# Kernel tuning notes

Hardware: AMD Instinct MI355X
Metric: run time of the kernel (lower is better)

## Reference

```python
import jax, jax.numpy as jnp
import numpy as np
import math

B, S, E, H = 2, 8192, 1024, 16
D = E // H  # 64
CHUNK = 128


def _build_slopes(n):
    # ALiBi-style slopes (n is a power of 2 here)
    start = 2.0 ** (-(2.0 ** -(math.log2(n) - 3)))
    return np.array([start * (start ** i) for i in range(n)], dtype=np.float32)


def setup_inputs() -> dict:
    key = jax.random.key(0)
    ks = jax.random.split(key, 6)
    x = jax.random.normal(ks[0], (B, S, E), dtype=jnp.float32)
    # rotary table: (S, D//2, 2) = (cos, sin)
    inv_freq = 1.0 / (10000.0 ** (np.arange(0, D, 2, dtype=np.float32) / D))
    ang = np.arange(S, dtype=np.float32)[:, None] * inv_freq[None, :]  # (S, D/2)
    freqs_cis = jnp.asarray(np.stack([np.cos(ang), np.sin(ang)], axis=-1))
    wq = jax.random.normal(ks[1], (E, E), dtype=jnp.float32) * 0.02
    wk = jax.random.normal(ks[2], (E, E), dtype=jnp.float32) * 0.02
    wv = jax.random.normal(ks[3], (E, E), dtype=jnp.float32) * 0.02
    wo = jax.random.normal(ks[4], (E, E), dtype=jnp.float32) * 0.02
    rms_w = jnp.ones((E,), dtype=jnp.float32)
    return {"x": x, "freqs_cis": freqs_cis, "wq": wq, "wk": wk, "wv": wv, "wo": wo, "rms_w": rms_w}


def apply_rotary(x, fc):
    # x: (b, s, h, d); fc: (s, d/2, 2)
    xr = x.reshape(*x.shape[:-1], -1, 2)          # (b,s,h,d/2,2)
    fc = fc[None, :, None, :, :]                   # (1,s,1,d/2,2)
    out = jnp.stack([
        xr[..., 0] * fc[..., 0] - xr[..., 1] * fc[..., 1],
        xr[..., 1] * fc[..., 0] + xr[..., 0] * fc[..., 1],
    ], axis=-1)
    return out.reshape(x.shape)


def lightning_attn(q, k, v, slopes, C=CHUNK):
    # q,k,v: (B,H,S,D); per-head decay lambda = exp(-slope)
    Bs, Hs, Ss, Ds = q.shape
    NC = Ss // C
    j = jnp.arange(C, dtype=jnp.float32)
    diff = j[:, None] - j[None, :]
    s3 = slopes[:, None, None]                     # (H,1,1)
    Dmask = jnp.where(diff >= 0, jnp.exp(-s3 * diff), 0.0)   # (H,C,C) intra decay
    q_dec = jnp.exp(-slopes[:, None] * (j + 1.0))             # (H,C) cross-chunk q decay
    k_dec = jnp.exp(-slopes[:, None] * (C - 1.0 - j))         # (H,C) state-update k decay
    c_dec = jnp.exp(-slopes * C)[None, :, None, None]         # (1,H,1,1) full-chunk decay
    qc = q.reshape(Bs, Hs, NC, C, Ds).transpose(2, 0, 1, 3, 4)
    kc = k.reshape(Bs, Hs, NC, C, Ds).transpose(2, 0, 1, 3, 4)
    vc = v.reshape(Bs, Hs, NC, C, Ds).transpose(2, 0, 1, 3, 4)

    def step(St, inp):
        qb, kb, vb = inp                                       # (B,H,C,D)
        scores = jnp.einsum('bhid,bhjd->bhij', qb, kb) * Dmask[None]
        o = jnp.einsum('bhij,bhjd->bhid', scores, vb)
        o = o + q_dec[None, :, :, None] * jnp.einsum('bhid,bhde->bhie', qb, St)
        St = c_dec * St + jnp.einsum('bhcd,bhce->bhde', kb * k_dec[None, :, :, None], vb)
        return St, o

    S0 = jnp.zeros((Bs, Hs, Ds, Ds), dtype=jnp.float32)
    _, oc = jax.lax.scan(step, S0, (qc, kc, vc))               # oc: (NC,B,H,C,D)
    return oc.transpose(1, 2, 0, 3, 4).reshape(Bs, Hs, Ss, Ds)


def rms_norm(x, w, eps=1e-5):
    xf = x.astype(jnp.float32)
    n = xf * jax.lax.rsqrt(jnp.mean(xf * xf, axis=-1, keepdims=True) + eps)
    return n.astype(x.dtype) * w


def reference(x, freqs_cis, wq, wk, wv, wo, rms_w):
    b, s, _ = x.shape
    slopes = jnp.asarray(_build_slopes(H))
    q = (x @ wq.T).reshape(b, s, H, D)
    k = (x @ wk.T).reshape(b, s, H, D)
    v = (x @ wv.T).reshape(b, s, H, D)
    q = apply_rotary(q, freqs_cis)
    k = apply_rotary(k, freqs_cis)
    q = q.transpose(0, 2, 1, 3)   # (B,H,S,D)
    k = k.transpose(0, 2, 1, 3)
    v = v.transpose(0, 2, 1, 3)
    o = lightning_attn(q, k, v, slopes)             # (B,H,S,D)
    o = o.transpose(0, 2, 1, 3).reshape(b, s, E)    # b n (h d)
    o = rms_norm(o, rms_w)
    return o @ wo.T
```

## Files before the change

kernel.cpp:

```cpp
#include <hip/hip_runtime.h>


using h16   = _Float16;
using h16x8 = __attribute__((ext_vector_type(8))) _Float16;
using h16x4 = __attribute__((ext_vector_type(4))) _Float16;
using f32x4 = __attribute__((ext_vector_type(4))) float;

#define MFMA16(a,b,c) __builtin_amdgcn_mfma_f32_16x16x32_f16(a,b,c,0,0,0)

#define GLOAD16(gp, lp) __builtin_amdgcn_global_load_lds( \
    (const __attribute__((address_space(1))) void*)(gp),  \
    (__attribute__((address_space(3))) void*)(lp), 16, 0, 0)

__device__ __forceinline__ h16x8 rope8(h16x8 v, const float* __restrict__ fp) {
  float4 f0 = *(const float4*)fp;
  float4 f1 = *(const float4*)(fp + 4);
  h16x8 o; float x0, x1;
  x0=(float)v[0]; x1=(float)v[1]; o[0]=(h16)(x0*f0.x - x1*f0.y); o[1]=(h16)(x1*f0.x + x0*f0.y);
  x0=(float)v[2]; x1=(float)v[3]; o[2]=(h16)(x0*f0.z - x1*f0.w); o[3]=(h16)(x1*f0.z + x0*f0.w);
  x0=(float)v[4]; x1=(float)v[5]; o[4]=(h16)(x0*f1.x - x1*f1.y); o[5]=(h16)(x1*f1.x + x0*f1.y);
  x0=(float)v[6]; x1=(float)v[7]; o[6]=(h16)(x0*f1.z - x1*f1.w); o[7]=(h16)(x1*f1.z + x0*f1.w);
  return o;
}

__global__ __launch_bounds__(256) void k_cvt(const float* __restrict__ s,
                                             h16* __restrict__ d, int n) {
  int i = (blockIdx.x * 256 + threadIdx.x) * 8;
  if (i >= n) return;
  float4 a = *(const float4*)(s + i);
  float4 b = *(const float4*)(s + i + 4);
  h16x8 o;
  o[0]=(h16)a.x; o[1]=(h16)a.y; o[2]=(h16)a.z; o[3]=(h16)a.w;
  o[4]=(h16)b.x; o[5]=(h16)b.y; o[6]=(h16)b.z; o[7]=(h16)b.w;
  *(h16x8*)(d + i) = o;
}

__device__ __forceinline__ void gemm256_loop(
    const h16* __restrict__ At, const h16* __restrict__ Bt,
    char* smem, int w, int l, f32x4 (&acc)[8][4])
{
  const int tid = w*64 + l;
  const int wr = w >> 2, wc = w & 3;

  size_t gof[2];
  #pragma unroll
  for (int c = 0; c < 2; c++) {
    int G = c*512 + tid;
    int pp = G >> 3;
    int idx = (G & 7) ^ (pp & 7);
    gof[c] = (size_t)(2*pp + (idx >> 2))*1024 + (idx & 3)*8;
  }

  const int q16 = ((((l & 1) << 2) | (l >> 4)) ^ ((l >> 1) & 7)) * 16;
  const int abyte = wr*8192 + ((l >> 1) & 7)*128 + q16;
  const int bbyte = 16384 + wc*4096 + ((l >> 1) & 7)*128 + q16;

  auto stageA = [&](int kt) {
    char* buf = smem + (kt & 3)*32768;
    #pragma unroll
    for (int c = 0; c < 2; c++)
      GLOAD16(At + gof[c] + kt*32, buf + c*8192 + w*1024);
  };
  auto stageB = [&](int kt) {
    char* buf = smem + (kt & 3)*32768;
    #pragma unroll
    for (int c = 0; c < 2; c++)
      GLOAD16(Bt + gof[c] + kt*32, buf + 16384 + c*8192 + w*1024);
  };

  stageA(0); stageB(0); stageA(1); stageB(1);
  asm volatile("s_waitcnt vmcnt(4)" ::: "memory");
  __builtin_amdgcn_sched_barrier(0);
  __builtin_amdgcn_s_barrier();

  for (int t = 0; t < 32; ++t) {
    const char* buf = smem + (t & 3)*32768;
    h16x8 af[8], bf[4];
    #pragma unroll
    for (int mf = 0; mf < 4; mf++) af[mf] = *(const h16x8*)(buf + abyte + mf*1024);
    #pragma unroll
    for (int nf = 0; nf < 4; nf++) bf[nf] = *(const h16x8*)(buf + bbyte + nf*1024);
    if (t < 30) stageA(t + 2);
    asm volatile("s_waitcnt lgkmcnt(0)" ::: "memory");
    __builtin_amdgcn_sched_barrier(0);
    __builtin_amdgcn_s_setprio(1);
    #pragma unroll
    for (int mf = 0; mf < 4; mf++)
      #pragma unroll
      for (int nf = 0; nf < 4; nf++)
        acc[mf][nf] = MFMA16(af[mf], bf[nf], acc[mf][nf]);
    __builtin_amdgcn_s_setprio(0);
    #pragma unroll
    for (int mf = 0; mf < 4; mf++) af[4+mf] = *(const h16x8*)(buf + abyte + 4096 + mf*1024);
    if (t < 30) stageB(t + 2);
    asm volatile("s_waitcnt lgkmcnt(0)" ::: "memory");
    __builtin_amdgcn_sched_barrier(0);
    __builtin_amdgcn_s_setprio(1);
    #pragma unroll
    for (int mf = 0; mf < 4; mf++)
      #pragma unroll
      for (int nf = 0; nf < 4; nf++)
        acc[4+mf][nf] = MFMA16(af[4+mf], bf[nf], acc[4+mf][nf]);
    __builtin_amdgcn_s_setprio(0);
    if (t < 30)       asm volatile("s_waitcnt vmcnt(4)" ::: "memory");
    else if (t == 30) asm volatile("s_waitcnt vmcnt(0)" ::: "memory");
    if (t < 31) {
      __builtin_amdgcn_sched_barrier(0);
      __builtin_amdgcn_s_barrier();
    }
  }
}

__global__ __launch_bounds__(512, 2) void k_qkv(
    const h16* __restrict__ xh, const h16* __restrict__ w3,
    h16* __restrict__ qn, h16* __restrict__ kn, h16* __restrict__ vn)
{
  extern __shared__ __align__(16) char smem[];
  const int tid = threadIdx.x;
  const int w = tid >> 6, l = tid & 63;
  const int m0 = blockIdx.x * 256;
  const int nt = blockIdx.y;
  const int wr = w >> 2, wc = w & 3;

  f32x4 acc[8][4] = {};
  gemm256_loop(xh + (size_t)m0*1024, w3 + (size_t)(nt*256)*1024, smem, w, l, acc);

  const int proj = nt >> 2;
  h16* dst = proj == 0 ? qn : (proj == 1 ? kn : vn);
  const int cb = (nt & 3)*256 + wc*64;
  #pragma unroll
  for (int mf = 0; mf < 8; mf++)
    #pragma unroll
    for (int nf = 0; nf < 4; nf++)
      #pragma unroll
      for (int r = 0; r < 4; r++) {
        int row = wr*128 + mf*16 + ((l >> 4) << 2) + r;
        int col = cb + nf*16 + (l & 15);
        dst[(size_t)(m0 + row)*1024 + col] = (h16)acc[mf][nf][r];
      }
}

__global__ __launch_bounds__(512, 2) void k_out(
    const h16* __restrict__ an, const h16* __restrict__ woh,
    float* __restrict__ out)
{
  extern __shared__ __align__(16) char smem[];
  const int tid = threadIdx.x;
  const int w = tid >> 6, l = tid & 63;
  const int m0 = blockIdx.x * 256;
  const int n0 = blockIdx.y * 256;
  const int wr = w >> 2, wc = w & 3;

  f32x4 acc[8][4] = {};
  gemm256_loop(an + (size_t)m0*1024, woh + (size_t)n0*1024, smem, w, l, acc);

  #pragma unroll
  for (int mf = 0; mf < 8; mf++)
    #pragma unroll
    for (int nf = 0; nf < 4; nf++)
      #pragma unroll
      for (int r = 0; r < 4; r++) {
        int row = wr*128 + mf*16 + ((l >> 4) << 2) + r;
        int col = n0 + wc*64 + nf*16 + (l & 15);
        out[(size_t)(m0 + row)*1024 + col] = acc[mf][nf][r];
      }
}

__global__ __launch_bounds__(256) void k_tr(
    const h16* __restrict__ kn, const h16* __restrict__ vn,
    const float* __restrict__ fc,
    h16* __restrict__ kts, h16* __restrict__ vt)
{
  __shared__ __align__(16) h16 tl[128*64];
  __shared__ float dt[128];
  const int tid = threadIdx.x;
  const int st = blockIdx.x;
  const int bh = blockIdx.y;
  const int b = bh >> 4, h = bh & 15;
  if (tid < 128) {
    float slope = exp2f(-0.5f * (float)(h + 1));
    dt[tid] = expf(-slope * (float)(127 - tid));
  }
  const size_t ibase = ((size_t)(b*8192 + st*128))*1024 + h*64;
  const size_t obase = (size_t)bh*64*8192 + st*128;
  const int cr = tid >> 3, c8 = tid & 7;

  for (int which = 0; which < 2; ++which) {
    const h16* src = which ? vn : kn;
    h16* dstp = which ? vt : kts;
    __syncthreads();
    #pragma unroll
    for (int i = 0; i < 4; i++) {
      int r = i*32 + cr;
      h16x8 v = *(const h16x8*)(src + ibase + (size_t)r*1024 + c8*8);
      if (!which) v = rope8(v, fc + (size_t)(st*128 + r)*64 + c8*8);
      int slot = (c8 + ((r >> 3) & 7)) & 7;
      *(h16x8*)(tl + r*64 + slot*8) = v;
    }
    __syncthreads();
    #pragma unroll
    for (int i = 0; i < 4; i++) {
      int chunk = i*256 + tid;
      int d = chunk >> 4;
      int j8 = chunk & 15;
      h16x8 o;
      #pragma unroll
      for (int jj = 0; jj < 8; jj++) {
        int c = j8*8 + jj;
        int pos = (d + ((c >> 3) & 7)*8) & 63;
        float fv = (float)tl[c*64 + pos];
        if (!which) fv *= dt[c];
        o[jj] = (h16)fv;
      }
      *(h16x8*)(dstp + obase + (size_t)d*8192 + j8*8) = o;
    }
  }
}

__global__ __launch_bounds__(256) void k_kv(
    const h16* __restrict__ kts, const h16* __restrict__ vt,
    float* __restrict__ T)
{
  const int tid = threadIdx.x;
  const int t = blockIdx.x;
  const int bh = blockIdx.y;
  const int w = tid >> 6, l = tid & 63;
  const h16* vb = vt  + (size_t)bh*64*8192 + t*128;
  const h16* kb = kts + (size_t)bh*64*8192 + t*128;
  f32x4 acc[4] = {};
  h16x8 a[4];
  #pragma unroll
  for (int ks = 0; ks < 4; ks++)
    a[ks] = *(const h16x8*)(vb + (size_t)(w*16 + (l & 15))*8192 + ks*32 + (l >> 4)*8);
  #pragma unroll
  for (int nf = 0; nf < 4; nf++) {
    #pragma unroll
    for (int ks = 0; ks < 4; ks++) {
      h16x8 bfr = *(const h16x8*)(kb + (size_t)(nf*16 + (l & 15))*8192 + ks*32 + (l >> 4)*8);
      acc[nf] = MFMA16(a[ks], bfr, acc[nf]);
    }
  }
  float* Tb = T + ((size_t)bh*64 + t)*4096;
  #pragma unroll
  for (int nf = 0; nf < 4; nf++)
    #pragma unroll
    for (int r = 0; r < 4; r++) {
      int e = w*16 + ((l >> 4) << 2) + r;
      int d = nf*16 + (l & 15);
      Tb[e*64 + d] = acc[nf][r];
    }
}

__global__ __launch_bounds__(256) void k_scan(const float* __restrict__ T,
                                              h16* __restrict__ ph) {
  const int bh = blockIdx.x;
  const int j  = blockIdx.y * 256 + threadIdx.x;
  const int h = bh & 15;
  const float cdec = expf(-exp2f(-0.5f*(float)(h+1)) * 128.0f);
  const float* Tb = T + (size_t)bh*64*4096 + j;
  h16* pb = ph + (size_t)bh*64*4096 + j;
  float run = 0.f;
  for (int t = 0; t < 64; t++) {
    float kv = Tb[(size_t)t*4096];
    pb[(size_t)t*4096] = (h16)run;
    run = cdec*run + kv;
  }
}

__global__ __launch_bounds__(256) void k_att(
    const h16* __restrict__ qn, const h16* __restrict__ kn,
    const float* __restrict__ fc,
    const h16* __restrict__ vt, const h16* __restrict__ ph,
    h16* __restrict__ oh)
{
  __shared__ __align__(16) h16 P[128*144];
  __shared__ float dt[128], qd[128];
  const int tid = threadIdx.x;
  const int t = blockIdx.x;
  const int bh = blockIdx.y;
  const int b = bh >> 4, h = bh & 15;
  if (tid < 128) {
    float slope = exp2f(-0.5f*(float)(h+1));
    dt[tid] = expf(-slope*(float)tid);
    qd[tid] = expf(-slope*(float)(tid+1));
  }
  __syncthreads();
  const int w = tid >> 6, l = tid & 63;
  const int iw = w * 32;
  const h16* qb = qn + ((size_t)(b*8192 + t*128))*1024 + h*64;
  const h16* kb = kn + ((size_t)(b*8192 + t*128))*1024 + h*64;
  const h16* vb = vt + (size_t)bh*64*8192 + t*128;
  const h16* pb = ph + ((size_t)bh*64 + t)*4096;
  const float* fcb = fc + (size_t)(t*128)*64;

  h16x8 aq[2][2];
  #pragma unroll
  for (int mf = 0; mf < 2; mf++)
    #pragma unroll
    for (int ks = 0; ks < 2; ks++) {
      int row = iw + mf*16 + (l & 15);
      int d0 = ks*32 + (l >> 4)*8;
      aq[mf][ks] = rope8(*(const h16x8*)(qb + (size_t)row*1024 + d0),
                         fcb + (size_t)row*64 + d0);
    }

  f32x4 sc[2][8] = {};
  #pragma unroll
  for (int nf = 0; nf < 8; nf++) {
    if (nf*16 <= iw + 31) {
      #pragma unroll
      for (int ks = 0; ks < 2; ks++) {
        int row = nf*16 + (l & 15);
        int d0 = ks*32 + (l >> 4)*8;
        h16x8 bk = rope8(*(const h16x8*)(kb + (size_t)row*1024 + d0),
                         fcb + (size_t)row*64 + d0);
        sc[0][nf] = MFMA16(aq[0][ks], bk, sc[0][nf]);
        sc[1][nf] = MFMA16(aq[1][ks], bk, sc[1][nf]);
      }
    }
  }
  #pragma unroll
  for (int mf = 0; mf < 2; mf++) {
    #pragma unroll
    for (int nf = 0; nf < 8; nf++) {
      #pragma unroll
      for (int r = 0; r < 4; r++) {
        int i = iw + mf*16 + ((l >> 4) << 2) + r;
        int j = nf*16 + (l & 15);
        int diff = i - j;
        float v = diff >= 0 ? sc[mf][nf][r]*dt[diff] : 0.f;
        P[i*144 + j] = (h16)v;
      }
    }
  }
  f32x4 ao[2][4] = {};
  #pragma unroll
  for (int kc = 0; kc < 4; kc++) {
    h16x8 ap0 = *(const h16x8*)(P + (size_t)(iw + (l & 15))*144 + kc*32 + (l >> 4)*8);
    h16x8 ap1 = *(const h16x8*)(P + (size_t)(iw + 16 + (l & 15))*144 + kc*32 + (l >> 4)*8);
    #pragma unroll
    for (int nf = 0; nf < 4; nf++) {
      h16x8 bv = *(const h16x8*)(vb + (size_t)(nf*16 + (l & 15))*8192 + kc*32 + (l >> 4)*8);
      ao[0][nf] = MFMA16(ap0, bv, ao[0][nf]);
      ao[1][nf] = MFMA16(ap1, bv, ao[1][nf]);
    }
  }
  f32x4 a2[2][4] = {};
  #pragma unroll
  for (int ks = 0; ks < 2; ks++) {
    #pragma unroll
    for (int nf = 0; nf < 4; nf++) {
      h16x8 bs = *(const h16x8*)(pb + (size_t)(nf*16 + (l & 15))*64 + ks*32 + (l >> 4)*8);
      a2[0][nf] = MFMA16(aq[0][ks], bs, a2[0][nf]);
      a2[1][nf] = MFMA16(aq[1][ks], bs, a2[1][nf]);
    }
  }
  #pragma unroll
  for (int mf = 0; mf < 2; mf++) {
    #pragma unroll
    for (int nf = 0; nf < 4; nf++) {
      #pragma unroll
      for (int r = 0; r < 4; r++) {
        int i = iw + mf*16 + ((l >> 4) << 2) + r;
        int e = nf*16 + (l & 15);
        float o = ao[mf][nf][r] + qd[i]*a2[mf][nf][r];
        int s = t*128 + i;
        oh[((size_t)(b*8192 + s))*1024 + h*64 + e] = (h16)o;
      }
    }
  }
}

__global__ __launch_bounds__(256) void k_rms(const h16* __restrict__ o,
                                             const float* __restrict__ rw,
                                             h16* __restrict__ an) {
  const int tid = threadIdx.x;
  const size_t base = (size_t)blockIdx.x * 1024;
  h16x4 hv = *(const h16x4*)(o + base + tid*4);
  float v0 = (float)hv[0], v1 = (float)hv[1], v2 = (float)hv[2], v3 = (float)hv[3];
  float ss = v0*v0 + v1*v1 + v2*v2 + v3*v3;
  #pragma unroll
  for (int off = 32; off > 0; off >>= 1) ss += __shfl_down(ss, off);
  __shared__ float red[4];
  if ((tid & 63) == 0) red[tid >> 6] = ss;
  __syncthreads();
  float f = rsqrtf((red[0]+red[1]+red[2]+red[3]) * (1.0f/1024.0f) + 1e-5f);
  float4 wv = *(const float4*)(rw + tid*4);
  h16x4 r;
  r[0] = (h16)(v0*f*wv.x); r[1] = (h16)(v1*f*wv.y);
  r[2] = (h16)(v2*f*wv.z); r[3] = (h16)(v3*f*wv.w);
  *(h16x4*)(an + base + tid*4) = r;
}

extern "C" void kernel_launch(void* const* d_in, const int* in_sizes, int n_in,
                              void* d_out, int out_size, void* d_ws, size_t ws_size,
                              hipStream_t stream) {
  const float* x  = (const float*)d_in[0];
  const float* fc = (const float*)d_in[1];
  const float* wq = (const float*)d_in[2];
  const float* wk = (const float*)d_in[3];
  const float* wv = (const float*)d_in[4];
  const float* wo = (const float*)d_in[5];
  const float* rw = (const float*)d_in[6];
  float* out = (float*)d_out;

  char* p = (char*)d_ws;
  const size_t SZ = 33554432;
  h16* xh  = (h16*)(p);
  h16* vn  = (h16*)(p + 3*SZ);
  h16* kts = (h16*)(p + 4*SZ);
  h16* vt  = (h16*)(p + 5*SZ);
  float* T = (float*)(p + 6*SZ);
  h16* w3  = (h16*)(p + 7*SZ);
  h16* woh = (h16*)(p + 7*SZ + 6291456);
  h16* qn = (h16*)out;
  h16* kn = (h16*)out + 16777216;

  (void)hipFuncSetAttribute((const void*)k_qkv, hipFuncAttributeMaxDynamicSharedMemorySize, 131072);
  (void)hipFuncSetAttribute((const void*)k_out, hipFuncAttributeMaxDynamicSharedMemorySize, 131072);

  hipLaunchKernelGGL(k_cvt, dim3(8192), dim3(256), 0, stream, x, xh, 16777216);
  hipLaunchKernelGGL(k_cvt, dim3(512), dim3(256), 0, stream, wq, w3, 1048576);
  hipLaunchKernelGGL(k_cvt, dim3(512), dim3(256), 0, stream, wk, w3 + 1048576, 1048576);
  hipLaunchKernelGGL(k_cvt, dim3(512), dim3(256), 0, stream, wv, w3 + 2097152, 1048576);
  hipLaunchKernelGGL(k_cvt, dim3(512), dim3(256), 0, stream, wo, woh, 1048576);

  hipLaunchKernelGGL(k_qkv, dim3(64, 12), dim3(512), 131072, stream, xh, w3, qn, kn, vn);
  hipLaunchKernelGGL(k_tr,  dim3(64, 32), dim3(256), 0, stream, kn, vn, fc, kts, vt);
  hipLaunchKernelGGL(k_kv,  dim3(64, 32), dim3(256), 0, stream, kts, vt, T);
  h16* ph = vn;
  hipLaunchKernelGGL(k_scan, dim3(32, 16), dim3(256), 0, stream, T, ph);
  h16* oh = (h16*)T;
  hipLaunchKernelGGL(k_att, dim3(64, 32), dim3(256), 0, stream, qn, kn, fc, vt, ph, oh);
  h16* an = xh;
  hipLaunchKernelGGL(k_rms, dim3(16384), dim3(256), 0, stream, oh, rw, an);
  hipLaunchKernelGGL(k_out, dim3(64, 4), dim3(512), 131072, stream, an, woh, out);
}
```

Before: 327.0 us.

## Fuse K/V transpose with chunk KV-state GEMM and merge weight conversions

```diff
diff --git a/kernel.cpp b/kernel.cpp
--- a/kernel.cpp
+++ b/kernel.cpp
@@ -35,6 +35,22 @@
   *(h16x8*)(d + i) = o;
 }
 
+__global__ __launch_bounds__(256) void k_cvt4(
+    const float* __restrict__ s0, const float* __restrict__ s1,
+    const float* __restrict__ s2, const float* __restrict__ s3,
+    h16* __restrict__ d0, h16* __restrict__ d1,
+    h16* __restrict__ d2, h16* __restrict__ d3) {
+  const float* s = blockIdx.y == 0 ? s0 : (blockIdx.y == 1 ? s1 : (blockIdx.y == 2 ? s2 : s3));
+  h16* d        = blockIdx.y == 0 ? d0 : (blockIdx.y == 1 ? d1 : (blockIdx.y == 2 ? d2 : d3));
+  int i = (blockIdx.x * 256 + threadIdx.x) * 8;
+  float4 a = *(const float4*)(s + i);
+  float4 b = *(const float4*)(s + i + 4);
+  h16x8 o;
+  o[0]=(h16)a.x; o[1]=(h16)a.y; o[2]=(h16)a.z; o[3]=(h16)a.w;
+  o[4]=(h16)b.x; o[5]=(h16)b.y; o[6]=(h16)b.z; o[7]=(h16)b.w;
+  *(h16x8*)(d + i) = o;
+}
+
 __device__ __forceinline__ void gemm256_loop(
     const h16* __restrict__ At, const h16* __restrict__ Bt,
     char* smem, int w, int l, f32x4 (&acc)[8][4])
@@ -166,12 +182,14 @@
       }
 }
 
-__global__ __launch_bounds__(256) void k_tr(
+__global__ __launch_bounds__(256) void k_trkv(
     const h16* __restrict__ kn, const h16* __restrict__ vn,
     const float* __restrict__ fc,
-    h16* __restrict__ kts, h16* __restrict__ vt)
+    h16* __restrict__ vt, h16* __restrict__ Th)
 {
   __shared__ __align__(16) h16 tl[128*64];
+  __shared__ __align__(16) h16 kT2[64*136];
+  __shared__ __align__(16) h16 vT2[64*136];
   __shared__ float dt[128];
   const int tid = threadIdx.x;
   const int st = blockIdx.x;
@@ -187,7 +205,7 @@
 
   for (int which = 0; which < 2; ++which) {
     const h16* src = which ? vn : kn;
-    h16* dstp = which ? vt : kts;
+    h16* dT2 = which ? vT2 : kT2;
     __syncthreads();
     #pragma unroll
     for (int i = 0; i < 4; i++) {
@@ -212,56 +230,48 @@
         if (!which) fv *= dt[c];
         o[jj] = (h16)fv;
       }
-      *(h16x8*)(dstp + obase + (size_t)d*8192 + j8*8) = o;
-    }
-  }
-}
-
-__global__ __launch_bounds__(256) void k_kv(
-    const h16* __restrict__ kts, const h16* __restrict__ vt,
-    float* __restrict__ T)
-{
-  const int tid = threadIdx.x;
-  const int t = blockIdx.x;
-  const int bh = blockIdx.y;
+      *(h16x8*)(dT2 + d*136 + j8*8) = o;
+      if (which) *(h16x8*)(vt + obase + (size_t)d*8192 + j8*8) = o;
+    }
+  }
+  __syncthreads();
+
   const int w = tid >> 6, l = tid & 63;
-  const h16* vb = vt  + (size_t)bh*64*8192 + t*128;
-  const h16* kb = kts + (size_t)bh*64*8192 + t*128;
   f32x4 acc[4] = {};
   h16x8 a[4];
   #pragma unroll
   for (int ks = 0; ks < 4; ks++)
-    a[ks] = *(const h16x8*)(vb + (size_t)(w*16 + (l & 15))*8192 + ks*32 + (l >> 4)*8);
+    a[ks] = *(const h16x8*)(vT2 + (w*16 + (l & 15))*136 + ks*32 + (l >> 4)*8);
   #pragma unroll
   for (int nf = 0; nf < 4; nf++) {
     #pragma unroll
     for (int ks = 0; ks < 4; ks++) {
-      h16x8 bfr = *(const h16x8*)(kb + (size_t)(nf*16 + (l & 15))*8192 + ks*32 + (l >> 4)*8);
+      h16x8 bfr = *(const h16x8*)(kT2 + (nf*16 + (l & 15))*136 + ks*32 + (l >> 4)*8);
       acc[nf] = MFMA16(a[ks], bfr, acc[nf]);
     }
   }
-  float* Tb = T + ((size_t)bh*64 + t)*4096;
+  h16* Tb = Th + ((size_t)bh*64 + st)*4096;
   #pragma unroll
   for (int nf = 0; nf < 4; nf++)
     #pragma unroll
     for (int r = 0; r < 4; r++) {
       int e = w*16 + ((l >> 4) << 2) + r;
       int d = nf*16 + (l & 15);
-      Tb[e*64 + d] = acc[nf][r];
-    }
-}
-
-__global__ __launch_bounds__(256) void k_scan(const float* __restrict__ T,
+      Tb[e*64 + d] = (h16)acc[nf][r];
+    }
+}
+
+__global__ __launch_bounds__(256) void k_scan(const h16* __restrict__ Th,
                                               h16* __restrict__ ph) {
   const int bh = blockIdx.x;
   const int j  = blockIdx.y * 256 + threadIdx.x;
   const int h = bh & 15;
   const float cdec = expf(-exp2f(-0.5f*(float)(h+1)) * 128.0f);
-  const float* Tb = T + (size_t)bh*64*4096 + j;
+  const h16* Tb = Th + (size_t)bh*64*4096 + j;
   h16* pb = ph + (size_t)bh*64*4096 + j;
   float run = 0.f;
   for (int t = 0; t < 64; t++) {
-    float kv = Tb[(size_t)t*4096];
+    float kv = (float)Tb[(size_t)t*4096];
     pb[(size_t)t*4096] = (h16)run;
     run = cdec*run + kv;
   }
@@ -408,9 +418,9 @@
   const size_t SZ = 33554432;
   h16* xh  = (h16*)(p);
   h16* vn  = (h16*)(p + 3*SZ);
-  h16* kts = (h16*)(p + 4*SZ);
+  h16* Th  = (h16*)(p + 4*SZ);
   h16* vt  = (h16*)(p + 5*SZ);
-  float* T = (float*)(p + 6*SZ);
+  h16* oh  = (h16*)(p + 6*SZ);
   h16* w3  = (h16*)(p + 7*SZ);
   h16* woh = (h16*)(p + 7*SZ + 6291456);
   h16* qn = (h16*)out;
@@ -420,17 +430,13 @@
   (void)hipFuncSetAttribute((const void*)k_out, hipFuncAttributeMaxDynamicSharedMemorySize, 131072);
 
   hipLaunchKernelGGL(k_cvt, dim3(8192), dim3(256), 0, stream, x, xh, 16777216);
-  hipLaunchKernelGGL(k_cvt, dim3(512), dim3(256), 0, stream, wq, w3, 1048576);
-  hipLaunchKernelGGL(k_cvt, dim3(512), dim3(256), 0, stream, wk, w3 + 1048576, 1048576);
-  hipLaunchKernelGGL(k_cvt, dim3(512), dim3(256), 0, stream, wv, w3 + 2097152, 1048576);
-  hipLaunchKernelGGL(k_cvt, dim3(512), dim3(256), 0, stream, wo, woh, 1048576);
+  hipLaunchKernelGGL(k_cvt4, dim3(512, 4), dim3(256), 0, stream,
+                     wq, wk, wv, wo, w3, w3 + 1048576, w3 + 2097152, woh);
 
   hipLaunchKernelGGL(k_qkv, dim3(64, 12), dim3(512), 131072, stream, xh, w3, qn, kn, vn);
-  hipLaunchKernelGGL(k_tr,  dim3(64, 32), dim3(256), 0, stream, kn, vn, fc, kts, vt);
-  hipLaunchKernelGGL(k_kv,  dim3(64, 32), dim3(256), 0, stream, kts, vt, T);
+  hipLaunchKernelGGL(k_trkv, dim3(64, 32), dim3(256), 0, stream, kn, vn, fc, vt, Th);
   h16* ph = vn;
-  hipLaunchKernelGGL(k_scan, dim3(32, 16), dim3(256), 0, stream, T, ph);
-  h16* oh = (h16*)T;
+  hipLaunchKernelGGL(k_scan, dim3(32, 16), dim3(256), 0, stream, Th, ph);
   hipLaunchKernelGGL(k_att, dim3(64, 32), dim3(256), 0, stream, qn, kn, fc, vt, ph, oh);
   h16* an = xh;
   hipLaunchKernelGGL(k_rms, dim3(16384), dim3(256), 0, stream, oh, rw, an);
```

After: 295.5 us. -9.6%, faster.
